# Kernel tuning notes

Hardware: AMD Instinct MI355X
Metric: run time of the kernel (lower is better)

## Reference

```python
import jax, jax.numpy as jnp
import numpy as np

D = 128      # d_model
H = 8        # nhead
DFF = 256    # dim_feedforward
S = 1000     # num sets
L = 90       # set size
N = S * L    # total tokens (lidar voxels + image patches)
VN = 45000   # voxel_num (lidar tokens)


def _ln(x, g, b, eps=1e-5):
    m = x.mean(-1, keepdims=True)
    v = ((x - m) ** 2).mean(-1, keepdims=True)
    return (x - m) / jnp.sqrt(v + eps) * g + b


def setup_inputs() -> dict:
    key = jax.random.key(0)
    ks = jax.random.split(key, 16)
    p = lambda k, sh: jax.random.normal(k, sh, jnp.float32) * 0.02
    inp = {
        "src": jax.random.normal(ks[0], (N, D), jnp.float32),
        "pos": jax.random.normal(ks[1], (N, D), jnp.float32),
        # every token appears exactly once across all sets (permutation)
        "set_voxel_inds": jax.random.permutation(ks[2], N).reshape(S, L).astype(jnp.int32),
        "set_voxel_masks": jnp.zeros((S, L), bool),
        "voxel_num": VN,
        # nn.MultiheadAttention params
        "in_proj_w": p(ks[3], (3 * D, D)), "in_proj_b": jnp.zeros((3 * D,), jnp.float32),
        "out_w": p(ks[4], (D, D)), "out_b": jnp.zeros((D,), jnp.float32),
        # image-branch FFN + norms
        "lin1_w": p(ks[5], (DFF, D)), "lin1_b": jnp.zeros((DFF,), jnp.float32),
        "lin2_w": p(ks[6], (D, DFF)), "lin2_b": jnp.zeros((D,), jnp.float32),
        "n1_g": jnp.ones((D,), jnp.float32), "n1_b": jnp.zeros((D,), jnp.float32),
        "n2_g": jnp.ones((D,), jnp.float32), "n2_b": jnp.zeros((D,), jnp.float32),
        # lidar-branch FFN + norms (split_ffn=True)
        "l_lin1_w": p(ks[7], (DFF, D)), "l_lin1_b": jnp.zeros((DFF,), jnp.float32),
        "l_lin2_w": p(ks[8], (D, DFF)), "l_lin2_b": jnp.zeros((D,), jnp.float32),
        "ln1_g": jnp.ones((D,), jnp.float32), "ln1_b": jnp.zeros((D,), jnp.float32),
        "ln2_g": jnp.ones((D,), jnp.float32), "ln2_b": jnp.zeros((D,), jnp.float32),
        # encoder-layer output norm
        "enc_g": jnp.ones((D,), jnp.float32), "enc_b": jnp.zeros((D,), jnp.float32),
    }
    return inp


def reference(src, pos, set_voxel_inds, set_voxel_masks, voxel_num,
              in_proj_w, in_proj_b, out_w, out_b,
              lin1_w, lin1_b, lin2_w, lin2_b, n1_g, n1_b, n2_g, n2_b,
              l_lin1_w, l_lin1_b, l_lin2_w, l_lin2_b, ln1_g, ln1_b, ln2_g, ln2_b,
              enc_g, enc_b):
    identity = src
    Sx, Lx = set_voxel_inds.shape
    d = src.shape[-1]
    dh = d // H

    # ---- gather sets ----
    sf = src[set_voxel_inds]              # [S, L, D]
    sp = pos[set_voxel_inds]              # [S, L, D]
    q = sf + sp
    k = sf + sp
    v = sf

    # ---- nn.MultiheadAttention (batch_first, eval mode) ----
    qp = q @ in_proj_w[:d].T + in_proj_b[:d]
    kp = k @ in_proj_w[d:2 * d].T + in_proj_b[d:2 * d]
    vp = v @ in_proj_w[2 * d:].T + in_proj_b[2 * d:]
    qh = qp.reshape(Sx, Lx, H, dh)
    kh = kp.reshape(Sx, Lx, H, dh)
    vh = vp.reshape(Sx, Lx, H, dh)
    scale = 1.0 / np.sqrt(dh).astype(np.float32)
    scores = jnp.einsum('sqhd,skhd->shqk', qh, kh) * scale
    scores = scores + jnp.where(set_voxel_masks[:, None, None, :], -1e9, 0.0)
    attn = jax.nn.softmax(scores, axis=-1)
    o = jnp.einsum('shqk,skhd->sqhd', attn, vh).reshape(Sx, Lx, d)
    src2 = o @ out_w.T + out_b            # [S, L, D]

    # ---- scatter back to per-token order (first-occurrence via flip trick) ----
    flat = set_voxel_inds.reshape(-1)
    ar = jnp.arange(flat.shape[0], dtype=flat.dtype)
    perm = jnp.zeros((src.shape[0],), flat.dtype).at[flat[::-1]].set(ar[::-1])
    src2 = src2.reshape(-1, d)[perm]      # [N, D]

    # ---- split FFN (lidar first voxel_num tokens, image rest) ----
    x = src + src2
    x = jnp.concatenate([_ln(x[:voxel_num], ln1_g, ln1_b),
                         _ln(x[voxel_num:], n1_g, n1_b)], axis=0)
    fl = jax.nn.relu(x[:voxel_num] @ l_lin1_w.T + l_lin1_b) @ l_lin2_w.T + l_lin2_b
    fi = jax.nn.relu(x[voxel_num:] @ lin1_w.T + lin1_b) @ lin2_w.T + lin2_b
    x = x + jnp.concatenate([fl, fi], axis=0)
    x = jnp.concatenate([_ln(x[:voxel_num], ln2_g, ln2_b),
                         _ln(x[voxel_num:], n2_g, n2_b)], axis=0)

    # ---- UniTR_EncoderLayer residual + final norm ----
    return _ln(x + identity, enc_g, enc_b)
```

## Files before the change

kernel.cpp:

```cpp
#include <hip/hip_runtime.h>
#include <hip/hip_bf16.h>
#include <cmath>

#define N_TOK 90000
#define DM 128
#define NH 8
#define DH 16
#define NS 1000
#define LS 90
#define LSP 96
#define DFF 256
#define VN 45000
#define NB_L 704
#define NB_I 704

typedef __attribute__((ext_vector_type(8))) short short8;
typedef __attribute__((ext_vector_type(4))) short short4_t;
typedef __attribute__((ext_vector_type(4))) float f32x4;

#define SWZ(row, byte) ((byte) ^ (((row) & 7) << 4))

__device__ __forceinline__ unsigned short f2bf(float f) {
  __hip_bfloat16 h = __float2bfloat16(f);
  union { __hip_bfloat16 h; unsigned short u; } c; c.h = h; return c.u;
}
__device__ __forceinline__ float bf2f(unsigned short u) {
  union { unsigned short u; __hip_bfloat16 h; } c; c.u = u; return __bfloat162float(c.h);
}

__global__ __launch_bounds__(256) void k_wconv(
    const float* __restrict__ a0, const float* __restrict__ a1,
    const float* __restrict__ a2, const float* __restrict__ a3,
    const float* __restrict__ a4, const float* __restrict__ a5,
    unsigned short* __restrict__ dst)
{
  int c = blockIdx.x * 256 + threadIdx.x;
  const float* s; int base, kkn, K;
  if      (c <  6144) { s = a0; base = 0;     kkn = 4; K = 128; }
  else if (c <  8192) { s = a1; base = 6144;  kkn = 4; K = 128; }
  else if (c < 12288) { s = a2; base = 8192;  kkn = 4; K = 128; }
  else if (c < 16384) { s = a3; base = 12288; kkn = 4; K = 128; }
  else if (c < 20480) { s = a4; base = 16384; kkn = 8; K = 256; }
  else                { s = a5; base = 20480; kkn = 8; K = 256; }
  int lc = c - base;
  int nt = lc / (kkn * 64);
  int rem = lc - nt * (kkn * 64);
  int kk = rem >> 6, l = rem & 63;
  int row = nt * 16 + (l & 15);
  int col = kk * 32 + (l >> 4) * 8;
  const float* sp = s + (size_t)row * K + col;
  short8 o;
  #pragma unroll
  for (int e = 0; e < 8; e++) o[e] = (short)f2bf(sp[e]);
  *(short8*)&dst[(size_t)c * 8] = o;
}

__global__ __launch_bounds__(512, 4) void k_set(
    const float* __restrict__ src, const float* __restrict__ pos,
    const int* __restrict__ inds, const unsigned char* __restrict__ masks,
    const unsigned short* __restrict__ Wq, const float* __restrict__ bq_,
    const unsigned short* __restrict__ Wo, const float* __restrict__ bo,
    const float* __restrict__ lg, const float* __restrict__ lb,
    const float* __restrict__ ig, const float* __restrict__ ib,
    unsigned short* __restrict__ x1)
{
  __shared__ __align__(16) char QKV[LSP * 256 + 128 * 200];
  __shared__ float bias[LSP];
  __shared__ int tok[LSP];
  const int s = blockIdx.x;
  const int tid = threadIdx.x;
  const int w = tid >> 6, l = tid & 63;
  const int g = l >> 4, cb = l & 15;

  char* Kd = QKV;
  char* Vt = QKV + LSP * 256;
  char* Qd = QKV + LSP * 256;

  const int row = w * 16 + cb;
  short8 bq[4];

  if (tid >= 384 && tid < 384 + LSP) {
    int i = tid - 384;
    tok[i] = inds[s * LS + ((i < LS) ? i : 0)];
    bias[i] = (i < LS && !masks[s * LS + i]) ? 0.f : -1e9f;
  }

  if (w < 6) {
    const int t = inds[s * LS + ((row < LS) ? row : 0)];
    short8 bv[4];
    #pragma unroll
    for (int kk = 0; kk < 4; kk++) {
      const float* sp = &src[(size_t)t * DM + kk * 32 + g * 8];
      const float* pp = &pos[(size_t)t * DM + kk * 32 + g * 8];
      float4 s0 = *(const float4*)sp, s1 = *(const float4*)(sp + 4);
      float4 p0 = *(const float4*)pp, p1 = *(const float4*)(pp + 4);
      short8 q, v;
      q[0] = (short)f2bf(s0.x + p0.x); q[1] = (short)f2bf(s0.y + p0.y);
      q[2] = (short)f2bf(s0.z + p0.z); q[3] = (short)f2bf(s0.w + p0.w);
      q[4] = (short)f2bf(s1.x + p1.x); q[5] = (short)f2bf(s1.y + p1.y);
      q[6] = (short)f2bf(s1.z + p1.z); q[7] = (short)f2bf(s1.w + p1.w);
      v[0] = (short)f2bf(s0.x); v[1] = (short)f2bf(s0.y);
      v[2] = (short)f2bf(s0.z); v[3] = (short)f2bf(s0.w);
      v[4] = (short)f2bf(s1.x); v[5] = (short)f2bf(s1.y);
      v[6] = (short)f2bf(s1.z); v[7] = (short)f2bf(s1.w);
      bq[kk] = q; bv[kk] = v;
    }

    #pragma unroll
    for (int nt = 16; nt < 24; nt++) {
      const unsigned short* wb = Wq + ((size_t)nt * 256 + l) * 8;
      short8 A[4];
      #pragma unroll
      for (int kk = 0; kk < 4; kk++) A[kk] = *(const short8*)(wb + kk * 512);
      f32x4 acc = {0.f, 0.f, 0.f, 0.f};
      #pragma unroll
      for (int kk = 0; kk < 4; kk++)
        acc = __builtin_amdgcn_mfma_f32_16x16x32_bf16(A[kk], bv[kk], acc, 0, 0, 0);
      float4 bb = *(const float4*)&bq_[nt * 16 + g * 4];
      float bba[4] = {bb.x, bb.y, bb.z, bb.w};
      #pragma unroll
      for (int j = 0; j < 4; j++) {
        int ch = (nt - 16) * 16 + g * 4 + j;
        *(unsigned short*)(Vt + ch * 200 + row * 2) = f2bf(acc[j] + bba[j]);
      }
    }

    #pragma unroll
    for (int nt = 8; nt < 16; nt++) {
      const unsigned short* wb = Wq + ((size_t)nt * 256 + l) * 8;
      short8 A[4];
      #pragma unroll
      for (int kk = 0; kk < 4; kk++) A[kk] = *(const short8*)(wb + kk * 512);
      f32x4 acc = {0.f, 0.f, 0.f, 0.f};
      #pragma unroll
      for (int kk = 0; kk < 4; kk++)
        acc = __builtin_amdgcn_mfma_f32_16x16x32_bf16(A[kk], bq[kk], acc, 0, 0, 0);
      float4 bb = *(const float4*)&bq_[nt * 16 + g * 4];
      const int colb = (nt & 7) * 16 + g * 4;
      short4_t o;
      o[0] = (short)f2bf(acc[0] + bb.x); o[1] = (short)f2bf(acc[1] + bb.y);
      o[2] = (short)f2bf(acc[2] + bb.z); o[3] = (short)f2bf(acc[3] + bb.w);
      *(short4_t*)(Kd + SWZ(row, row * 256 + colb * 2)) = o;
    }
  }
  __syncthreads();

  short8 aV[3];
  #pragma unroll
  for (int kb = 0; kb < 3; kb++) {
    const char* vr = Vt + (w * 16 + cb) * 200;
    short4_t lo = *(const short4_t*)(vr + (kb * 32 + g * 4) * 2);
    short4_t hi = *(const short4_t*)(vr + (kb * 32 + 16 + g * 4) * 2);
    short8 v;
    v[0] = lo[0]; v[1] = lo[1]; v[2] = lo[2]; v[3] = lo[3];
    v[4] = hi[0]; v[5] = hi[1]; v[6] = hi[2]; v[7] = hi[3];
    aV[kb] = v;
  }
  __syncthreads();

  if (w < 6) {
    #pragma unroll
    for (int nt = 0; nt < 8; nt++) {
      const unsigned short* wb = Wq + ((size_t)nt * 256 + l) * 8;
      short8 A[4];
      #pragma unroll
      for (int kk = 0; kk < 4; kk++) A[kk] = *(const short8*)(wb + kk * 512);
      f32x4 acc = {0.f, 0.f, 0.f, 0.f};
      #pragma unroll
      for (int kk = 0; kk < 4; kk++)
        acc = __builtin_amdgcn_mfma_f32_16x16x32_bf16(A[kk], bq[kk], acc, 0, 0, 0);
      float4 bb = *(const float4*)&bq_[nt * 16 + g * 4];
      const int colb = nt * 16 + g * 4;
      short4_t o;
      o[0] = (short)f2bf(acc[0] + bb.x); o[1] = (short)f2bf(acc[1] + bb.y);
      o[2] = (short)f2bf(acc[2] + bb.z); o[3] = (short)f2bf(acc[3] + bb.w);
      *(short4_t*)(Qd + SWZ(row, row * 256 + colb * 2)) = o;
    }
  }
  __syncthreads();

  {
    const int hb = w * 32;
    float bi[6][4];
    #pragma unroll
    for (int kt = 0; kt < 6; kt++)
      #pragma unroll
      for (int r = 0; r < 4; r++)
        bi[kt][r] = bias[kt * 16 + g * 4 + r];

    short8 aK[6];
    #pragma unroll
    for (int kt = 0; kt < 6; kt++) {
      short8 v = {0, 0, 0, 0, 0, 0, 0, 0};
      int key = kt * 16 + cb;
      if (g < 2) v = *(const short8*)(Kd + SWZ(key, key * 256 + hb + g * 16));
      aK[kt] = v;
    }

    #pragma unroll
    for (int qt = 0; qt < 6; qt++) {
      const int qi = qt * 16 + cb;
      short8 aQ = {0, 0, 0, 0, 0, 0, 0, 0};
      if (g < 2) aQ = *(const short8*)(Qd + SWZ(qi, qi * 256 + hb + g * 16));

      f32x4 acc[6];
      #pragma unroll
      for (int kt = 0; kt < 6; kt++) {
        f32x4 z = {0.f, 0.f, 0.f, 0.f};
        acc[kt] = __builtin_amdgcn_mfma_f32_16x16x32_bf16(aK[kt], aQ, z, 0, 0, 0);
      }
      #pragma unroll
      for (int kt = 0; kt < 6; kt++)
        #pragma unroll
        for (int r = 0; r < 4; r++)
          acc[kt][r] = acc[kt][r] * 0.25f + bi[kt][r];
      float mx = -1e30f;
      #pragma unroll
      for (int kt = 0; kt < 6; kt++)
        #pragma unroll
        for (int r = 0; r < 4; r++) mx = fmaxf(mx, acc[kt][r]);
      mx = fmaxf(mx, __shfl_xor(mx, 16));
      mx = fmaxf(mx, __shfl_xor(mx, 32));
      float sm = 0.f;
      #pragma unroll
      for (int kt = 0; kt < 6; kt++)
        #pragma unroll
        for (int r = 0; r < 4; r++) {
          acc[kt][r] = __expf(acc[kt][r] - mx);
          sm += acc[kt][r];
        }
      sm += __shfl_xor(sm, 16);
      sm += __shfl_xor(sm, 32);
      const float inv = 1.f / sm;
      f32x4 accO = {0.f, 0.f, 0.f, 0.f};
      #pragma unroll
      for (int kb = 0; kb < 3; kb++) {
        short8 p;
        #pragma unroll
        for (int e = 0; e < 8; e++) {
          int kt = kb * 2 + (e >> 2);
          p[e] = (short)f2bf(acc[kt][e & 3] * inv);
        }
        accO = __builtin_amdgcn_mfma_f32_16x16x32_bf16(aV[kb], p, accO, 0, 0, 0);
      }
      if (qi < LS) {
        short4_t o;
        #pragma unroll
        for (int r = 0; r < 4; r++) o[r] = (short)f2bf(accO[r]);
        *(short4_t*)(Qd + SWZ(qi, qi * 256 + hb + g * 8)) = o;
      }
    }
  }
  __syncthreads();

  if (w < 6) {
    const bool ok = row < LS;
    const int t = tok[row];
    short8 bf[4];
    #pragma unroll
    for (int kk = 0; kk < 4; kk++)
      bf[kk] = *(const short8*)(Qd + SWZ(row, row * 256 + kk * 64 + g * 16));

    float ta[8][4]; float ssum = 0.f;
    #pragma unroll
    for (int nt = 0; nt < 8; nt++) {
      const unsigned short* wb = Wo + ((size_t)nt * 256 + l) * 8;
      short8 A[4];
      #pragma unroll
      for (int kk = 0; kk < 4; kk++) A[kk] = *(const short8*)(wb + kk * 512);
      f32x4 c = {0.f, 0.f, 0.f, 0.f};
      #pragma unroll
      for (int kk = 0; kk < 4; kk++)
        c = __builtin_amdgcn_mfma_f32_16x16x32_bf16(A[kk], bf[kk], c, 0, 0, 0);
      float4 bo4 = *(const float4*)&bo[nt * 16 + g * 4];
      float4 sv  = *(const float4*)&src[(size_t)t * DM + nt * 16 + g * 4];
      ta[nt][0] = c[0] + bo4.x + sv.x;
      ta[nt][1] = c[1] + bo4.y + sv.y;
      ta[nt][2] = c[2] + bo4.z + sv.z;
      ta[nt][3] = c[3] + bo4.w + sv.w;
      ssum += ta[nt][0] + ta[nt][1] + ta[nt][2] + ta[nt][3];
    }
    ssum += __shfl_xor(ssum, 16); ssum += __shfl_xor(ssum, 32);
    const float mean = ssum * (1.f / 128.f);
    float vv = 0.f;
    #pragma unroll
    for (int nt = 0; nt < 8; nt++)
      #pragma unroll
      for (int j = 0; j < 4; j++) { float d = ta[nt][j] - mean; vv += d * d; }
    vv += __shfl_xor(vv, 16); vv += __shfl_xor(vv, 32);
    const float rstd = rsqrtf(vv * (1.f / 128.f) + 1e-5f);
    const bool lidar = t < VN;
    const float* gp = lidar ? lg : ig;
    const float* bp = lidar ? lb : ib;
    #pragma unroll
    for (int nt = 0; nt < 8; nt++) {
      float4 g4 = *(const float4*)&gp[nt * 16 + g * 4];
      float4 b4 = *(const float4*)&bp[nt * 16 + g * 4];
      short4_t o;
      o[0] = (short)f2bf((ta[nt][0] - mean) * rstd * g4.x + b4.x);
      o[1] = (short)f2bf((ta[nt][1] - mean) * rstd * g4.y + b4.y);
      o[2] = (short)f2bf((ta[nt][2] - mean) * rstd * g4.z + b4.z);
      o[3] = (short)f2bf((ta[nt][3] - mean) * rstd * g4.w + b4.w);
      if (ok) *(short4_t*)&x1[(size_t)t * DM + nt * 16 + g * 4] = o;
    }
  }
}

__global__ __launch_bounds__(256) void k_ffn(
    const unsigned short* __restrict__ x1, const float* __restrict__ src,
    const unsigned short* __restrict__ W1l, const float* __restrict__ B1l,
    const unsigned short* __restrict__ W1i, const float* __restrict__ B1i,
    const unsigned short* __restrict__ W2l, const float* __restrict__ B2l,
    const unsigned short* __restrict__ W2i, const float* __restrict__ B2i,
    const float* __restrict__ lg2, const float* __restrict__ lbb2,
    const float* __restrict__ ig2, const float* __restrict__ ibb2,
    const float* __restrict__ eg, const float* __restrict__ eb,
    float* __restrict__ out)
{
  __shared__ __align__(16) unsigned short hid[64 * 256];
  const int tid = threadIdx.x;
  const int w = tid >> 6, l = tid & 63;
  const int g = l >> 4, cb = l & 15;
  const bool lid = blockIdx.x < NB_L;
  const int t0 = lid ? blockIdx.x * 64 : VN + (blockIdx.x - NB_L) * 64;
  const int limit = lid ? VN : N_TOK;
  const unsigned short* W1 = lid ? W1l : W1i;
  const float* B1 = lid ? B1l : B1i;
  const unsigned short* W2 = lid ? W2l : W2i;
  const float* B2 = lid ? B2l : B2i;
  const float* g2  = lid ? lg2  : ig2;
  const float* bb2 = lid ? lbb2 : ibb2;

  const int row = w * 16 + cb;
  const int t = t0 + row;
  const int tc = (t < limit) ? t : (limit - 1);
  const bool ok = t < limit;

  short8 b1[4];
  #pragma unroll
  for (int kk = 0; kk < 4; kk++)
    b1[kk] = *(const short8*)&x1[(size_t)tc * DM + kk * 32 + g * 8];

  for (int nt = 0; nt < 16; nt++) {
    const unsigned short* wbase = W1 + ((size_t)nt * 256 + l) * 8;
    short8 A[4];
    #pragma unroll
    for (int kk = 0; kk < 4; kk++) A[kk] = *(const short8*)(wbase + kk * 512);
    f32x4 acc = {0.f, 0.f, 0.f, 0.f};
    #pragma unroll
    for (int kk = 0; kk < 4; kk++)
      acc = __builtin_amdgcn_mfma_f32_16x16x32_bf16(A[kk], b1[kk], acc, 0, 0, 0);
    float4 bb = *(const float4*)&B1[nt * 16 + g * 4];
    short4_t h;
    h[0] = (short)f2bf(fmaxf(acc[0] + bb.x, 0.f));
    h[1] = (short)f2bf(fmaxf(acc[1] + bb.y, 0.f));
    h[2] = (short)f2bf(fmaxf(acc[2] + bb.z, 0.f));
    h[3] = (short)f2bf(fmaxf(acc[3] + bb.w, 0.f));
    *(short4_t*)((char*)hid + SWZ(row, row * 512 + nt * 32 + g * 8)) = h;
  }

  short8 b2[8];
  #pragma unroll
  for (int kk = 0; kk < 8; kk++)
    b2[kk] = *(const short8*)((const char*)hid + SWZ(row, row * 512 + kk * 64 + g * 16));

  f32x4 acc2[8];
  for (int nt = 0; nt < 8; nt++) {
    const unsigned short* wbase = W2 + ((size_t)nt * 512 + l) * 8;
    short8 A[8];
    #pragma unroll
    for (int kk = 0; kk < 8; kk++) A[kk] = *(const short8*)(wbase + kk * 512);
    f32x4 c = {0.f, 0.f, 0.f, 0.f};
    #pragma unroll
    for (int kk = 0; kk < 8; kk++)
      c = __builtin_amdgcn_mfma_f32_16x16x32_bf16(A[kk], b2[kk], c, 0, 0, 0);
    acc2[nt] = c;
  }

  float ta[8][4]; float s = 0.f;
  #pragma unroll
  for (int nt = 0; nt < 8; nt++) {
    short4_t xv = *(const short4_t*)&x1[(size_t)tc * DM + nt * 16 + g * 4];
    float4 bb = *(const float4*)&B2[nt * 16 + g * 4];
    ta[nt][0] = bf2f((unsigned short)xv[0]) + acc2[nt][0] + bb.x;
    ta[nt][1] = bf2f((unsigned short)xv[1]) + acc2[nt][1] + bb.y;
    ta[nt][2] = bf2f((unsigned short)xv[2]) + acc2[nt][2] + bb.z;
    ta[nt][3] = bf2f((unsigned short)xv[3]) + acc2[nt][3] + bb.w;
    s += ta[nt][0] + ta[nt][1] + ta[nt][2] + ta[nt][3];
  }
  s += __shfl_xor(s, 16); s += __shfl_xor(s, 32);
  const float mean = s * (1.f / 128.f);
  float vv = 0.f;
  #pragma unroll
  for (int nt = 0; nt < 8; nt++)
    #pragma unroll
    for (int j = 0; j < 4; j++) { float d = ta[nt][j] - mean; vv += d * d; }
  vv += __shfl_xor(vv, 16); vv += __shfl_xor(vv, 32);
  const float rstd = rsqrtf(vv * (1.f / 128.f) + 1e-5f);

  float za[8][4]; float s2 = 0.f;
  #pragma unroll
  for (int nt = 0; nt < 8; nt++) {
    float4 g4 = *(const float4*)&g2[nt * 16 + g * 4];
    float4 b4 = *(const float4*)&bb2[nt * 16 + g * 4];
    float4 sv = *(const float4*)&src[(size_t)tc * DM + nt * 16 + g * 4];
    za[nt][0] = (ta[nt][0] - mean) * rstd * g4.x + b4.x + sv.x;
    za[nt][1] = (ta[nt][1] - mean) * rstd * g4.y + b4.y + sv.y;
    za[nt][2] = (ta[nt][2] - mean) * rstd * g4.z + b4.z + sv.z;
    za[nt][3] = (ta[nt][3] - mean) * rstd * g4.w + b4.w + sv.w;
    s2 += za[nt][0] + za[nt][1] + za[nt][2] + za[nt][3];
  }
  s2 += __shfl_xor(s2, 16); s2 += __shfl_xor(s2, 32);
  const float mean2 = s2 * (1.f / 128.f);
  float vv2 = 0.f;
  #pragma unroll
  for (int nt = 0; nt < 8; nt++)
    #pragma unroll
    for (int j = 0; j < 4; j++) { float d = za[nt][j] - mean2; vv2 += d * d; }
  vv2 += __shfl_xor(vv2, 16); vv2 += __shfl_xor(vv2, 32);
  const float rstd2 = rsqrtf(vv2 * (1.f / 128.f) + 1e-5f);

  #pragma unroll
  for (int nt = 0; nt < 8; nt++) {
    float4 e4 = *(const float4*)&eg[nt * 16 + g * 4];
    float4 eb4 = *(const float4*)&eb[nt * 16 + g * 4];
    float4 o;
    o.x = (za[nt][0] - mean2) * rstd2 * e4.x + eb4.x;
    o.y = (za[nt][1] - mean2) * rstd2 * e4.y + eb4.y;
    o.z = (za[nt][2] - mean2) * rstd2 * e4.z + eb4.z;
    o.w = (za[nt][3] - mean2) * rstd2 * e4.w + eb4.w;
    if (ok) *(float4*)&out[(size_t)t * DM + nt * 16 + g * 4] = o;
  }
}

extern "C" void kernel_launch(void* const* d_in, const int* in_sizes, int n_in,
                              void* d_out, int out_size, void* d_ws, size_t ws_size,
                              hipStream_t stream) {
  (void)in_sizes; (void)n_in; (void)out_size;
  const float* src  = (const float*)d_in[0];
  const float* pos  = (const float*)d_in[1];
  const int*   inds = (const int*)d_in[2];
  const unsigned char* masks = (const unsigned char*)d_in[3];
  const float* Wqkv = (const float*)d_in[5];
  const float* bqkv = (const float*)d_in[6];
  const float* Wo   = (const float*)d_in[7];
  const float* bo   = (const float*)d_in[8];
  const float* lin1_w = (const float*)d_in[9];
  const float* lin1_b = (const float*)d_in[10];
  const float* lin2_w = (const float*)d_in[11];
  const float* lin2_b = (const float*)d_in[12];
  const float* n1_g = (const float*)d_in[13];
  const float* n1_b = (const float*)d_in[14];
  const float* n2_g = (const float*)d_in[15];
  const float* n2_b = (const float*)d_in[16];
  const float* l_lin1_w = (const float*)d_in[17];
  const float* l_lin1_b = (const float*)d_in[18];
  const float* l_lin2_w = (const float*)d_in[19];
  const float* l_lin2_b = (const float*)d_in[20];
  const float* ln1_g = (const float*)d_in[21];
  const float* ln1_b = (const float*)d_in[22];
  const float* ln2_g = (const float*)d_in[23];
  const float* ln2_b = (const float*)d_in[24];
  const float* enc_g = (const float*)d_in[25];
  const float* enc_b = (const float*)d_in[26];

  const size_t buf = (size_t)N_TOK * DM;
  if (ws_size < (buf + 196608) * sizeof(unsigned short)) return;
  unsigned short* x1  = (unsigned short*)d_ws;
  unsigned short* Wbf = x1 + buf;
  unsigned short* WbQKV = Wbf;
  unsigned short* WbO   = Wbf + 6144  * 8;
  unsigned short* Wb1L  = Wbf + 8192  * 8;
  unsigned short* Wb1I  = Wbf + 12288 * 8;
  unsigned short* Wb2L  = Wbf + 16384 * 8;
  unsigned short* Wb2I  = Wbf + 20480 * 8;

  k_wconv<<<96, 256, 0, stream>>>(Wqkv, Wo, l_lin1_w, lin1_w, l_lin2_w, lin2_w, Wbf);
  k_set<<<NS, 512, 0, stream>>>(src, pos, inds, masks, WbQKV, bqkv, WbO, bo,
                                ln1_g, ln1_b, n1_g, n1_b, x1);
  k_ffn<<<NB_L + NB_I, 256, 0, stream>>>(x1, src,
                                         Wb1L, l_lin1_b, Wb1I, lin1_b,
                                         Wb2L, l_lin2_b, Wb2I, lin2_b,
                                         ln2_g, ln2_b, n2_g, n2_b,
                                         enc_g, enc_b, (float*)d_out);
}
```

Measured before the change: 135.9 us.

## Split fused per-set attention kernel into token-order QKV, attention, and out-proj kernels

```diff
diff --git a/kernel.cpp b/kernel.cpp
--- a/kernel.cpp
+++ b/kernel.cpp
@@ -13,6 +13,7 @@
 #define VN 45000
 #define NB_L 704
 #define NB_I 704
+#define NBQ 1407
 
 typedef __attribute__((ext_vector_type(8))) short short8;
 typedef __attribute__((ext_vector_type(4))) short short4_t;
@@ -55,254 +56,239 @@
   *(short8*)&dst[(size_t)c * 8] = o;
 }
 
-__global__ __launch_bounds__(512, 4) void k_set(
+__global__ __launch_bounds__(256) void k_qkv(
     const float* __restrict__ src, const float* __restrict__ pos,
+    const unsigned short* __restrict__ Wq, const float* __restrict__ bq_,
+    unsigned short* __restrict__ qkv)
+{
+  const int tid = threadIdx.x;
+  const int w = tid >> 6, l = tid & 63;
+  const int g = l >> 4, cb = l & 15;
+  const int row = w * 16 + cb;
+  const int t = blockIdx.x * 64 + row;
+  const int tc = (t < N_TOK) ? t : (N_TOK - 1);
+  const bool ok = t < N_TOK;
+
+  short8 bq[4], bv[4];
+  #pragma unroll
+  for (int kk = 0; kk < 4; kk++) {
+    const float* sp = &src[(size_t)tc * DM + kk * 32 + g * 8];
+    const float* pp = &pos[(size_t)tc * DM + kk * 32 + g * 8];
+    float4 s0 = *(const float4*)sp, s1 = *(const float4*)(sp + 4);
+    float4 p0 = *(const float4*)pp, p1 = *(const float4*)(pp + 4);
+    short8 q, v;
+    q[0] = (short)f2bf(s0.x + p0.x); q[1] = (short)f2bf(s0.y + p0.y);
+    q[2] = (short)f2bf(s0.z + p0.z); q[3] = (short)f2bf(s0.w + p0.w);
+    q[4] = (short)f2bf(s1.x + p1.x); q[5] = (short)f2bf(s1.y + p1.y);
+    q[6] = (short)f2bf(s1.z + p1.z); q[7] = (short)f2bf(s1.w + p1.w);
+    v[0] = (short)f2bf(s0.x); v[1] = (short)f2bf(s0.y);
+    v[2] = (short)f2bf(s0.z); v[3] = (short)f2bf(s0.w);
+    v[4] = (short)f2bf(s1.x); v[5] = (short)f2bf(s1.y);
+    v[6] = (short)f2bf(s1.z); v[7] = (short)f2bf(s1.w);
+    bq[kk] = q; bv[kk] = v;
+  }
+
+  #pragma unroll
+  for (int nt = 0; nt < 16; nt++) {
+    const unsigned short* wb = Wq + ((size_t)nt * 256 + l) * 8;
+    short8 A[4];
+    #pragma unroll
+    for (int kk = 0; kk < 4; kk++) A[kk] = *(const short8*)(wb + kk * 512);
+    f32x4 acc = {0.f, 0.f, 0.f, 0.f};
+    #pragma unroll
+    for (int kk = 0; kk < 4; kk++)
+      acc = __builtin_amdgcn_mfma_f32_16x16x32_bf16(A[kk], bq[kk], acc, 0, 0, 0);
+    float4 bb = *(const float4*)&bq_[nt * 16 + g * 4];
+    short4_t o;
+    o[0] = (short)f2bf(acc[0] + bb.x); o[1] = (short)f2bf(acc[1] + bb.y);
+    o[2] = (short)f2bf(acc[2] + bb.z); o[3] = (short)f2bf(acc[3] + bb.w);
+    if (ok) *(short4_t*)&qkv[(size_t)t * 384 + nt * 16 + g * 4] = o;
+  }
+  #pragma unroll
+  for (int nt = 16; nt < 24; nt++) {
+    const unsigned short* wb = Wq + ((size_t)nt * 256 + l) * 8;
+    short8 A[4];
+    #pragma unroll
+    for (int kk = 0; kk < 4; kk++) A[kk] = *(const short8*)(wb + kk * 512);
+    f32x4 acc = {0.f, 0.f, 0.f, 0.f};
+    #pragma unroll
+    for (int kk = 0; kk < 4; kk++)
+      acc = __builtin_amdgcn_mfma_f32_16x16x32_bf16(A[kk], bv[kk], acc, 0, 0, 0);
+    float4 bb = *(const float4*)&bq_[nt * 16 + g * 4];
+    short4_t o;
+    o[0] = (short)f2bf(acc[0] + bb.x); o[1] = (short)f2bf(acc[1] + bb.y);
+    o[2] = (short)f2bf(acc[2] + bb.z); o[3] = (short)f2bf(acc[3] + bb.w);
+    if (ok) *(short4_t*)&qkv[(size_t)t * 384 + nt * 16 + g * 4] = o;
+  }
+}
+
+__global__ __launch_bounds__(128) void k_attn(
+    const unsigned short* __restrict__ qkv,
     const int* __restrict__ inds, const unsigned char* __restrict__ masks,
-    const unsigned short* __restrict__ Wq, const float* __restrict__ bq_,
+    unsigned short* __restrict__ obuf)
+{
+  __shared__ int tok[LSP];
+  __shared__ float bias[LSP];
+  const int blk = blockIdx.x;
+  const int s = blk >> 2, hp = blk & 3;
+  const int tid = threadIdx.x;
+  const int w = tid >> 6, l = tid & 63;
+  const int g = l >> 4, cb = l & 15;
+  const int h = hp * 2 + w;
+
+  if (tid < LSP) {
+    tok[tid] = inds[s * LS + ((tid < LS) ? tid : 0)];
+    bias[tid] = (tid < LS && !masks[s * LS + tid]) ? 0.f : -1e9f;
+  }
+  __syncthreads();
+
+  short8 aK[6];
+  #pragma unroll
+  for (int kt = 0; kt < 6; kt++) {
+    short8 v = {0, 0, 0, 0, 0, 0, 0, 0};
+    if (g < 2) {
+      const int t = tok[kt * 16 + cb];
+      v = *(const short8*)&qkv[(size_t)t * 384 + 128 + h * 16 + g * 8];
+    }
+    aK[kt] = v;
+  }
+  short8 aV[3];
+  #pragma unroll
+  for (int kb = 0; kb < 3; kb++) {
+    short8 v;
+    #pragma unroll
+    for (int e = 0; e < 4; e++) {
+      const int t0 = tok[kb * 32 + g * 4 + e];
+      const int t1 = tok[kb * 32 + 16 + g * 4 + e];
+      v[e]     = (short)qkv[(size_t)t0 * 384 + 256 + h * 16 + cb];
+      v[e + 4] = (short)qkv[(size_t)t1 * 384 + 256 + h * 16 + cb];
+    }
+    aV[kb] = v;
+  }
+  float bi[6][4];
+  #pragma unroll
+  for (int kt = 0; kt < 6; kt++)
+    #pragma unroll
+    for (int r = 0; r < 4; r++)
+      bi[kt][r] = bias[kt * 16 + g * 4 + r];
+
+  #pragma unroll
+  for (int qt = 0; qt < 6; qt++) {
+    const int qi = qt * 16 + cb;
+    const int tq = tok[qi];
+    short8 aQ = {0, 0, 0, 0, 0, 0, 0, 0};
+    if (g < 2) aQ = *(const short8*)&qkv[(size_t)tq * 384 + h * 16 + g * 8];
+
+    f32x4 acc[6];
+    #pragma unroll
+    for (int kt = 0; kt < 6; kt++) {
+      f32x4 z = {0.f, 0.f, 0.f, 0.f};
+      acc[kt] = __builtin_amdgcn_mfma_f32_16x16x32_bf16(aK[kt], aQ, z, 0, 0, 0);
+    }
+    #pragma unroll
+    for (int kt = 0; kt < 6; kt++)
+      #pragma unroll
+      for (int r = 0; r < 4; r++)
+        acc[kt][r] = acc[kt][r] * 0.25f + bi[kt][r];
+    float mx = -1e30f;
+    #pragma unroll
+    for (int kt = 0; kt < 6; kt++)
+      #pragma unroll
+      for (int r = 0; r < 4; r++) mx = fmaxf(mx, acc[kt][r]);
+    mx = fmaxf(mx, __shfl_xor(mx, 16));
+    mx = fmaxf(mx, __shfl_xor(mx, 32));
+    float sm = 0.f;
+    #pragma unroll
+    for (int kt = 0; kt < 6; kt++)
+      #pragma unroll
+      for (int r = 0; r < 4; r++) {
+        acc[kt][r] = __expf(acc[kt][r] - mx);
+        sm += acc[kt][r];
+      }
+    sm += __shfl_xor(sm, 16);
+    sm += __shfl_xor(sm, 32);
+    const float inv = 1.f / sm;
+    f32x4 accO = {0.f, 0.f, 0.f, 0.f};
+    #pragma unroll
+    for (int kb = 0; kb < 3; kb++) {
+      short8 p;
+      #pragma unroll
+      for (int e = 0; e < 8; e++) {
+        int kt = kb * 2 + (e >> 2);
+        p[e] = (short)f2bf(acc[kt][e & 3] * inv);
+      }
+      accO = __builtin_amdgcn_mfma_f32_16x16x32_bf16(aV[kb], p, accO, 0, 0, 0);
+    }
+    if (qi < LS) {
+      short4_t o;
+      #pragma unroll
+      for (int r = 0; r < 4; r++) o[r] = (short)f2bf(accO[r]);
+      *(short4_t*)&obuf[(size_t)tq * DM + h * 16 + g * 4] = o;
+    }
+  }
+}
+
+__global__ __launch_bounds__(256) void k_oproj(
+    const unsigned short* __restrict__ obuf, const float* __restrict__ src,
     const unsigned short* __restrict__ Wo, const float* __restrict__ bo,
     const float* __restrict__ lg, const float* __restrict__ lb,
     const float* __restrict__ ig, const float* __restrict__ ib,
     unsigned short* __restrict__ x1)
 {
-  __shared__ __align__(16) char QKV[LSP * 256 + 128 * 200];
-  __shared__ float bias[LSP];
-  __shared__ int tok[LSP];
-  const int s = blockIdx.x;
   const int tid = threadIdx.x;
   const int w = tid >> 6, l = tid & 63;
   const int g = l >> 4, cb = l & 15;
-
-  char* Kd = QKV;
-  char* Vt = QKV + LSP * 256;
-  char* Qd = QKV + LSP * 256;
-
   const int row = w * 16 + cb;
-  short8 bq[4];
-
-  if (tid >= 384 && tid < 384 + LSP) {
-    int i = tid - 384;
-    tok[i] = inds[s * LS + ((i < LS) ? i : 0)];
-    bias[i] = (i < LS && !masks[s * LS + i]) ? 0.f : -1e9f;
-  }
-
-  if (w < 6) {
-    const int t = inds[s * LS + ((row < LS) ? row : 0)];
-    short8 bv[4];
-    #pragma unroll
-    for (int kk = 0; kk < 4; kk++) {
-      const float* sp = &src[(size_t)t * DM + kk * 32 + g * 8];
-      const float* pp = &pos[(size_t)t * DM + kk * 32 + g * 8];
-      float4 s0 = *(const float4*)sp, s1 = *(const float4*)(sp + 4);
-      float4 p0 = *(const float4*)pp, p1 = *(const float4*)(pp + 4);
-      short8 q, v;
-      q[0] = (short)f2bf(s0.x + p0.x); q[1] = (short)f2bf(s0.y + p0.y);
-      q[2] = (short)f2bf(s0.z + p0.z); q[3] = (short)f2bf(s0.w + p0.w);
-      q[4] = (short)f2bf(s1.x + p1.x); q[5] = (short)f2bf(s1.y + p1.y);
-      q[6] = (short)f2bf(s1.z + p1.z); q[7] = (short)f2bf(s1.w + p1.w);
-      v[0] = (short)f2bf(s0.x); v[1] = (short)f2bf(s0.y);
-      v[2] = (short)f2bf(s0.z); v[3] = (short)f2bf(s0.w);
-      v[4] = (short)f2bf(s1.x); v[5] = (short)f2bf(s1.y);
-      v[6] = (short)f2bf(s1.z); v[7] = (short)f2bf(s1.w);
-      bq[kk] = q; bv[kk] = v;
-    }
-
-    #pragma unroll
-    for (int nt = 16; nt < 24; nt++) {
-      const unsigned short* wb = Wq + ((size_t)nt * 256 + l) * 8;
-      short8 A[4];
-      #pragma unroll
-      for (int kk = 0; kk < 4; kk++) A[kk] = *(const short8*)(wb + kk * 512);
-      f32x4 acc = {0.f, 0.f, 0.f, 0.f};
-      #pragma unroll
-      for (int kk = 0; kk < 4; kk++)
-        acc = __builtin_amdgcn_mfma_f32_16x16x32_bf16(A[kk], bv[kk], acc, 0, 0, 0);
-      float4 bb = *(const float4*)&bq_[nt * 16 + g * 4];
-      float bba[4] = {bb.x, bb.y, bb.z, bb.w};
-      #pragma unroll
-      for (int j = 0; j < 4; j++) {
-        int ch = (nt - 16) * 16 + g * 4 + j;
-        *(unsigned short*)(Vt + ch * 200 + row * 2) = f2bf(acc[j] + bba[j]);
-      }
-    }
-
-    #pragma unroll
-    for (int nt = 8; nt < 16; nt++) {
-      const unsigned short* wb = Wq + ((size_t)nt * 256 + l) * 8;
-      short8 A[4];
-      #pragma unroll
-      for (int kk = 0; kk < 4; kk++) A[kk] = *(const short8*)(wb + kk * 512);
-      f32x4 acc = {0.f, 0.f, 0.f, 0.f};
-      #pragma unroll
-      for (int kk = 0; kk < 4; kk++)
-        acc = __builtin_amdgcn_mfma_f32_16x16x32_bf16(A[kk], bq[kk], acc, 0, 0, 0);
-      float4 bb = *(const float4*)&bq_[nt * 16 + g * 4];
-      const int colb = (nt & 7) * 16 + g * 4;
-      short4_t o;
-      o[0] = (short)f2bf(acc[0] + bb.x); o[1] = (short)f2bf(acc[1] + bb.y);
-      o[2] = (short)f2bf(acc[2] + bb.z); o[3] = (short)f2bf(acc[3] + bb.w);
-      *(short4_t*)(Kd + SWZ(row, row * 256 + colb * 2)) = o;
-    }
-  }
-  __syncthreads();
-
-  short8 aV[3];
-  #pragma unroll
-  for (int kb = 0; kb < 3; kb++) {
-    const char* vr = Vt + (w * 16 + cb) * 200;
-    short4_t lo = *(const short4_t*)(vr + (kb * 32 + g * 4) * 2);
-    short4_t hi = *(const short4_t*)(vr + (kb * 32 + 16 + g * 4) * 2);
-    short8 v;
-    v[0] = lo[0]; v[1] = lo[1]; v[2] = lo[2]; v[3] = lo[3];
-    v[4] = hi[0]; v[5] = hi[1]; v[6] = hi[2]; v[7] = hi[3];
-    aV[kb] = v;
-  }
-  __syncthreads();
-
-  if (w < 6) {
-    #pragma unroll
-    for (int nt = 0; nt < 8; nt++) {
-      const unsigned short* wb = Wq + ((size_t)nt * 256 + l) * 8;
-      short8 A[4];
-      #pragma unroll
-      for (int kk = 0; kk < 4; kk++) A[kk] = *(const short8*)(wb + kk * 512);
-      f32x4 acc = {0.f, 0.f, 0.f, 0.f};
-      #pragma unroll
-      for (int kk = 0; kk < 4; kk++)
-        acc = __builtin_amdgcn_mfma_f32_16x16x32_bf16(A[kk], bq[kk], acc, 0, 0, 0);
-      float4 bb = *(const float4*)&bq_[nt * 16 + g * 4];
-      const int colb = nt * 16 + g * 4;
-      short4_t o;
-      o[0] = (short)f2bf(acc[0] + bb.x); o[1] = (short)f2bf(acc[1] + bb.y);
-      o[2] = (short)f2bf(acc[2] + bb.z); o[3] = (short)f2bf(acc[3] + bb.w);
-      *(short4_t*)(Qd + SWZ(row, row * 256 + colb * 2)) = o;
-    }
-  }
-  __syncthreads();
-
-  {
-    const int hb = w * 32;
-    float bi[6][4];
-    #pragma unroll
-    for (int kt = 0; kt < 6; kt++)
-      #pragma unroll
-      for (int r = 0; r < 4; r++)
-        bi[kt][r] = bias[kt * 16 + g * 4 + r];
-
-    short8 aK[6];
-    #pragma unroll
-    for (int kt = 0; kt < 6; kt++) {
-      short8 v = {0, 0, 0, 0, 0, 0, 0, 0};
-      int key = kt * 16 + cb;
-      if (g < 2) v = *(const short8*)(Kd + SWZ(key, key * 256 + hb + g * 16));
-      aK[kt] = v;
-    }
-
-    #pragma unroll
-    for (int qt = 0; qt < 6; qt++) {
-      const int qi = qt * 16 + cb;
-      short8 aQ = {0, 0, 0, 0, 0, 0, 0, 0};
-      if (g < 2) aQ = *(const short8*)(Qd + SWZ(qi, qi * 256 + hb + g * 16));
-
-      f32x4 acc[6];
-      #pragma unroll
-      for (int kt = 0; kt < 6; kt++) {
-        f32x4 z = {0.f, 0.f, 0.f, 0.f};
-        acc[kt] = __builtin_amdgcn_mfma_f32_16x16x32_bf16(aK[kt], aQ, z, 0, 0, 0);
-      }
-      #pragma unroll
-      for (int kt = 0; kt < 6; kt++)
-        #pragma unroll
-        for (int r = 0; r < 4; r++)
-          acc[kt][r] = acc[kt][r] * 0.25f + bi[kt][r];
-      float mx = -1e30f;
-      #pragma unroll
-      for (int kt = 0; kt < 6; kt++)
-        #pragma unroll
-        for (int r = 0; r < 4; r++) mx = fmaxf(mx, acc[kt][r]);
-      mx = fmaxf(mx, __shfl_xor(mx, 16));
-      mx = fmaxf(mx, __shfl_xor(mx, 32));
-      float sm = 0.f;
-      #pragma unroll
-      for (int kt = 0; kt < 6; kt++)
-        #pragma unroll
-        for (int r = 0; r < 4; r++) {
-          acc[kt][r] = __expf(acc[kt][r] - mx);
-          sm += acc[kt][r];
-        }
-      sm += __shfl_xor(sm, 16);
-      sm += __shfl_xor(sm, 32);
-      const float inv = 1.f / sm;
-      f32x4 accO = {0.f, 0.f, 0.f, 0.f};
-      #pragma unroll
-      for (int kb = 0; kb < 3; kb++) {
-        short8 p;
-        #pragma unroll
-        for (int e = 0; e < 8; e++) {
-          int kt = kb * 2 + (e >> 2);
-          p[e] = (short)f2bf(acc[kt][e & 3] * inv);
-        }
-        accO = __builtin_amdgcn_mfma_f32_16x16x32_bf16(aV[kb], p, accO, 0, 0, 0);
-      }
-      if (qi < LS) {
-        short4_t o;
-        #pragma unroll
-        for (int r = 0; r < 4; r++) o[r] = (short)f2bf(accO[r]);
-        *(short4_t*)(Qd + SWZ(qi, qi * 256 + hb + g * 8)) = o;
-      }
-    }
-  }
-  __syncthreads();
-
-  if (w < 6) {
-    const bool ok = row < LS;
-    const int t = tok[row];
-    short8 bf[4];
+  const int t = blockIdx.x * 64 + row;
+  const int tc = (t < N_TOK) ? t : (N_TOK - 1);
+  const bool ok = t < N_TOK;
+
+  short8 b0[4];
+  #pragma unroll
+  for (int kk = 0; kk < 4; kk++)
+    b0[kk] = *(const short8*)&obuf[(size_t)tc * DM + kk * 32 + g * 8];
+
+  float ta[8][4]; float ssum = 0.f;
+  #pragma unroll
+  for (int nt = 0; nt < 8; nt++) {
+    const unsigned short* wb = Wo + ((size_t)nt * 256 + l) * 8;
+    short8 A[4];
+    #pragma unroll
+    for (int kk = 0; kk < 4; kk++) A[kk] = *(const short8*)(wb + kk * 512);
+    f32x4 c = {0.f, 0.f, 0.f, 0.f};
     #pragma unroll
     for (int kk = 0; kk < 4; kk++)
-      bf[kk] = *(const short8*)(Qd + SWZ(row, row * 256 + kk * 64 + g * 16));
-
-    float ta[8][4]; float ssum = 0.f;
-    #pragma unroll
-    for (int nt = 0; nt < 8; nt++) {
-      const unsigned short* wb = Wo + ((size_t)nt * 256 + l) * 8;
-      short8 A[4];
-      #pragma unroll
-      for (int kk = 0; kk < 4; kk++) A[kk] = *(const short8*)(wb + kk * 512);
-      f32x4 c = {0.f, 0.f, 0.f, 0.f};
-      #pragma unroll
-      for (int kk = 0; kk < 4; kk++)
-        c = __builtin_amdgcn_mfma_f32_16x16x32_bf16(A[kk], bf[kk], c, 0, 0, 0);
-      float4 bo4 = *(const float4*)&bo[nt * 16 + g * 4];
-      float4 sv  = *(const float4*)&src[(size_t)t * DM + nt * 16 + g * 4];
-      ta[nt][0] = c[0] + bo4.x + sv.x;
-      ta[nt][1] = c[1] + bo4.y + sv.y;
-      ta[nt][2] = c[2] + bo4.z + sv.z;
-      ta[nt][3] = c[3] + bo4.w + sv.w;
-      ssum += ta[nt][0] + ta[nt][1] + ta[nt][2] + ta[nt][3];
-    }
-    ssum += __shfl_xor(ssum, 16); ssum += __shfl_xor(ssum, 32);
-    const float mean = ssum * (1.f / 128.f);
-    float vv = 0.f;
-    #pragma unroll
-    for (int nt = 0; nt < 8; nt++)
-      #pragma unroll
-      for (int j = 0; j < 4; j++) { float d = ta[nt][j] - mean; vv += d * d; }
-    vv += __shfl_xor(vv, 16); vv += __shfl_xor(vv, 32);
-    const float rstd = rsqrtf(vv * (1.f / 128.f) + 1e-5f);
-    const bool lidar = t < VN;
-    const float* gp = lidar ? lg : ig;
-    const float* bp = lidar ? lb : ib;
-    #pragma unroll
-    for (int nt = 0; nt < 8; nt++) {
-      float4 g4 = *(const float4*)&gp[nt * 16 + g * 4];
-      float4 b4 = *(const float4*)&bp[nt * 16 + g * 4];
-      short4_t o;
-      o[0] = (short)f2bf((ta[nt][0] - mean) * rstd * g4.x + b4.x);
-      o[1] = (short)f2bf((ta[nt][1] - mean) * rstd * g4.y + b4.y);
-      o[2] = (short)f2bf((ta[nt][2] - mean) * rstd * g4.z + b4.z);
-      o[3] = (short)f2bf((ta[nt][3] - mean) * rstd * g4.w + b4.w);
-      if (ok) *(short4_t*)&x1[(size_t)t * DM + nt * 16 + g * 4] = o;
-    }
+      c = __builtin_amdgcn_mfma_f32_16x16x32_bf16(A[kk], b0[kk], c, 0, 0, 0);
+    float4 bo4 = *(const float4*)&bo[nt * 16 + g * 4];
+    float4 sv  = *(const float4*)&src[(size_t)tc * DM + nt * 16 + g * 4];
+    ta[nt][0] = c[0] + bo4.x + sv.x;
+    ta[nt][1] = c[1] + bo4.y + sv.y;
+    ta[nt][2] = c[2] + bo4.z + sv.z;
+    ta[nt][3] = c[3] + bo4.w + sv.w;
+    ssum += ta[nt][0] + ta[nt][1] + ta[nt][2] + ta[nt][3];
+  }
+  ssum += __shfl_xor(ssum, 16); ssum += __shfl_xor(ssum, 32);
+  const float mean = ssum * (1.f / 128.f);
+  float vv = 0.f;
+  #pragma unroll
+  for (int nt = 0; nt < 8; nt++)
+    #pragma unroll
+    for (int j = 0; j < 4; j++) { float d = ta[nt][j] - mean; vv += d * d; }
+  vv += __shfl_xor(vv, 16); vv += __shfl_xor(vv, 32);
+  const float rstd = rsqrtf(vv * (1.f / 128.f) + 1e-5f);
+  const bool lidar = tc < VN;
+  const float* gp = lidar ? lg : ig;
+  const float* bp = lidar ? lb : ib;
+  #pragma unroll
+  for (int nt = 0; nt < 8; nt++) {
+    float4 g4 = *(const float4*)&gp[nt * 16 + g * 4];
+    float4 b4 = *(const float4*)&bp[nt * 16 + g * 4];
+    short4_t o;
+    o[0] = (short)f2bf((ta[nt][0] - mean) * rstd * g4.x + b4.x);
+    o[1] = (short)f2bf((ta[nt][1] - mean) * rstd * g4.y + b4.y);
+    o[2] = (short)f2bf((ta[nt][2] - mean) * rstd * g4.z + b4.z);
+    o[3] = (short)f2bf((ta[nt][3] - mean) * rstd * g4.w + b4.w);
+    if (ok) *(short4_t*)&x1[(size_t)t * DM + nt * 16 + g * 4] = o;
   }
 }
 
@@ -464,10 +450,13 @@
   const float* enc_g = (const float*)d_in[25];
   const float* enc_b = (const float*)d_in[26];
 
-  const size_t buf = (size_t)N_TOK * DM;
-  if (ws_size < (buf + 196608) * sizeof(unsigned short)) return;
-  unsigned short* x1  = (unsigned short*)d_ws;
-  unsigned short* Wbf = x1 + buf;
+  const size_t nObuf = (size_t)N_TOK * DM;
+  const size_t nQkv  = (size_t)N_TOK * 384;
+  if (ws_size < (nObuf + nQkv + 196608) * sizeof(unsigned short)) return;
+  unsigned short* obuf = (unsigned short*)d_ws;
+  unsigned short* qkvb = obuf + nObuf;
+  unsigned short* x1   = qkvb;
+  unsigned short* Wbf  = qkvb + nQkv;
   unsigned short* WbQKV = Wbf;
   unsigned short* WbO   = Wbf + 6144  * 8;
   unsigned short* Wb1L  = Wbf + 8192  * 8;
@@ -476,8 +465,10 @@
   unsigned short* Wb2I  = Wbf + 20480 * 8;
 
   k_wconv<<<96, 256, 0, stream>>>(Wqkv, Wo, l_lin1_w, lin1_w, l_lin2_w, lin2_w, Wbf);
-  k_set<<<NS, 512, 0, stream>>>(src, pos, inds, masks, WbQKV, bqkv, WbO, bo,
-                                ln1_g, ln1_b, n1_g, n1_b, x1);
+  k_qkv<<<NBQ, 256, 0, stream>>>(src, pos, WbQKV, bqkv, qkvb);
+  k_attn<<<NS * 4, 128, 0, stream>>>(qkvb, inds, masks, obuf);
+  k_oproj<<<NBQ, 256, 0, stream>>>(obuf, src, WbO, bo,
+                                   ln1_g, ln1_b, n1_g, n1_b, x1);
   k_ffn<<<NB_L + NB_I, 256, 0, stream>>>(x1, src,
                                          Wb1L, l_lin1_b, Wb1I, lin1_b,
                                          Wb2L, l_lin2_b, Wb2I, lin2_b,
```

Result: slower. 175.0 us (+28.8%).
